# Performance work log

Measured on AMD Instinct MI355X. Metric: run time of the kernel, lower is better.

Reference implementation:

```python
import jax, jax.numpy as jnp
import numpy as np

N = 200000
C = 256
RATIO = 0.5
K = max(int(N * RATIO), 1)  # 100000 clusters kept


def setup_inputs() -> dict:
    key = jax.random.key(0)
    k1, k2, k3, k4 = jax.random.split(key, 4)
    x = jax.random.normal(k1, (N, C), dtype=jnp.float32)
    edge_index = jax.random.randint(k2, (2, N), 0, N, dtype=jnp.int32)  # E == N (source requires it)
    batch = jnp.zeros((N,), dtype=jnp.int32)
    # nn.Linear(C, 1): weight [1, C] -> flattened to [C]; bias [1] -> scalar
    w = jax.random.normal(k3, (C,), dtype=jnp.float32) * (1.0 / np.sqrt(C))
    b = jax.random.normal(k4, (1,), dtype=jnp.float32) * 0.01
    return {"x": x, "edge_index": edge_index, "batch": batch, "w": w, "b": b}


def reference(x, edge_index, batch, w, b):
    # scores = tanh(Linear(x)) over nodes: [N]
    scores = jnp.tanh(x @ w + b[0])
    # top-k node selection (torch uses sorted=False; ordering within topk is unspecified,
    # we use lax.top_k's sorted-descending order deterministically)
    _, perm = jax.lax.top_k(scores, K)  # [K] int32
    x_pool = x[perm]                    # [K, C]
    # mask is True for NON-selected nodes (as in the source)
    mask = jnp.ones((N,), dtype=bool).at[perm].set(False)
    # exactly N-K True entries (perm indices are distinct) -> static shape
    keep = jnp.nonzero(mask, size=N - K)[0]  # positions into edge rows (E == N)
    # relabel map: old node id -> new pooled id (0 for dropped nodes, as in source)
    new_mask = jnp.zeros((N,), dtype=jnp.int32).at[perm].set(jnp.arange(K, dtype=jnp.int32))
    ei = new_mask[edge_index[0][keep]]
    ej = new_mask[edge_index[1][keep]]
    edge_index_pool = jnp.stack([ei, ej], axis=0)  # [2, N-K]
    batch_pool = batch[perm]
    return (x_pool, edge_index_pool, perm, batch_pool, scores[perm])
```

## Files before the change

kernel.cpp:

```cpp
#include <hip/hip_runtime.h>

typedef unsigned long long u64;
typedef unsigned int u32;

#define NN 200000
#define CC 256
#define KK 100000
#define TILE 2048
#define NB ((NN + TILE - 1) / TILE)

#define OFF_X     0
#define OFF_E0    25600000
#define OFF_E1    25700000
#define OFF_PERM  25800000
#define OFF_BATCH 25900000
#define OFF_SC    26000000

__device__ __forceinline__ u32 key_of_f32(float s) {
    u32 b = __float_as_uint(s);
    u32 u = b ^ ((b & 0x80000000u) ? 0xFFFFFFFFu : 0x80000000u);
    return ~u;
}

__device__ __forceinline__ float xla_tanhf(float x) {
    const float kMax = (float)7.90531110763549805;
    float xc = fminf(fmaxf(x, -kMax), kMax);
    float x2 = __fmul_rn(xc, xc);
    float p = (float)-2.76076847742355e-16;
    p = __fadd_rn(__fmul_rn(p, x2), (float)2.00018790482477e-13);
    p = __fadd_rn(__fmul_rn(p, x2), (float)-8.60467152213735e-11);
    p = __fadd_rn(__fmul_rn(p, x2), (float)5.12229709037114e-08);
    p = __fadd_rn(__fmul_rn(p, x2), (float)1.48572235717979e-05);
    p = __fadd_rn(__fmul_rn(p, x2), (float)6.37261928875436e-04);
    p = __fadd_rn(__fmul_rn(p, x2), (float)4.89352455891786e-03);
    float num = __fmul_rn(xc, p);
    float q = (float)1.19825839466702e-06;
    q = __fadd_rn(__fmul_rn(q, x2), (float)1.18534705686654e-04);
    q = __fadd_rn(__fmul_rn(q, x2), (float)2.26843463243900e-03);
    q = __fadd_rn(__fmul_rn(q, x2), (float)4.89352518554385e-03);
    float t = __fdiv_rn(num, q);
    return (fabsf(x) < 0.0004f) ? x : t;
}

__global__ void score_kernel(const float* __restrict__ x, const float* __restrict__ w,
                             const float* __restrict__ b, u32* __restrict__ keys,
                             u32* __restrict__ vals, float* __restrict__ scoreF) {
    int i = (int)(blockIdx.x * blockDim.x + threadIdx.x);
    if (i >= NN) return;
    const float4* row = (const float4*)(x + (size_t)i * CC);
    const float4* wv  = (const float4*)w;
    float c0 = 0.f, c1 = 0.f, c2 = 0.f, c3 = 0.f;
    float c4 = 0.f, c5 = 0.f, c6 = 0.f, c7 = 0.f;
#pragma unroll 8
    for (int t = 0; t < 32; ++t) {
        float4 a0 = row[2 * t], a1 = row[2 * t + 1];
        float4 w0 = wv[2 * t],  w1 = wv[2 * t + 1];
        c0 = __builtin_fmaf(a0.x, w0.x, c0);
        c1 = __builtin_fmaf(a0.y, w0.y, c1);
        c2 = __builtin_fmaf(a0.z, w0.z, c2);
        c3 = __builtin_fmaf(a0.w, w0.w, c3);
        c4 = __builtin_fmaf(a1.x, w1.x, c4);
        c5 = __builtin_fmaf(a1.y, w1.y, c5);
        c6 = __builtin_fmaf(a1.z, w1.z, c6);
        c7 = __builtin_fmaf(a1.w, w1.w, c7);
    }
    float d0 = __fadd_rn(c0, c1);
    float d1 = __fadd_rn(c2, c3);
    float d2 = __fadd_rn(c4, c5);
    float d3 = __fadd_rn(c6, c7);
    float e0 = __fadd_rn(d0, d1);
    float e1 = __fadd_rn(d2, d3);
    float dot = __fadd_rn(e0, e1);
    float z = __fadd_rn(dot, b[0]);
    float s = xla_tanhf(z);
    keys[i]   = key_of_f32(s);
    keys[i]   = key_of_f32(s);
    vals[i]   = (u32)i;
    scoreF[i] = s;
}


__global__ void radix_count(const u32* __restrict__ keys, int shift,
                            u32* __restrict__ counts , int n) {
    __shared__ u32 hist[256];
    hist[threadIdx.x] = 0;
    __syncthreads();
    int wv = threadIdx.x >> 6, lane = threadIdx.x & 63;
    int base = blockIdx.x * TILE + wv * 512;
#pragma unroll
    for (int e = 0; e < 8; ++e) {
        int i = base + e * 64 + lane;
        if (i < n) {
            u32 d = (keys[i] >> shift) & 255u;
            atomicAdd(&hist[d], 1u);
        }
    }
    __syncthreads();
    counts[blockIdx.x * 256 + threadIdx.x] = hist[threadIdx.x];
}

template<bool ZMARK>
__global__ void radix_scatter(const u32* __restrict__ keysIn, const u32* __restrict__ valsIn,
                              u32* __restrict__ keysOut, u32* __restrict__ valsOut,
                              int shift, const u32* __restrict__ counts,
                              int* __restrict__ mark, int n) {
    __shared__ u32 waveCnt[4][256];
    __shared__ u32 scanbuf[256];
    __shared__ u32 tot[256];
    int tid = threadIdx.x;
    int wv = tid >> 6, lane = tid & 63;
    int myb = blockIdx.x;

    u32 myprefix = 0, total = 0;
#pragma unroll 7
    for (int bb = 0; bb < NB; ++bb) {
        u32 c = counts[bb * 256 + tid];
        if (bb < myb) myprefix += c;
        total += c;
    }
    tot[tid] = total;
    scanbuf[tid] = total;
#pragma unroll
    for (int w = 0; w < 4; ++w) waveCnt[w][tid] = 0;
    __syncthreads();
#pragma unroll
    for (int off = 1; off < 256; off <<= 1) {
        u32 v = (tid >= off) ? scanbuf[tid - off] : 0u;
        __syncthreads();
        scanbuf[tid] += v;
        __syncthreads();
    }
    u32 globalBase = (scanbuf[tid] - tot[tid]) + myprefix;

    int base = myb * TILE + wv * 512;
    u32 k[8];
    u64 peers[8];
    u32 dg[8];
    int valid[8];
#pragma unroll
    for (int e = 0; e < 8; ++e) {
        int i = base + e * 64 + lane;
        valid[e] = (i < n);
        k[e] = valid[e] ? keysIn[i] : 0u;
        dg[e] = (k[e] >> shift) & 255u;
        if (ZMARK && valid[e]) mark[i] = 0;
    }
#pragma unroll
    for (int e = 0; e < 8; ++e) {
        u64 mask = __ballot(valid[e]);
#pragma unroll
        for (int bit = 0; bit < 8; ++bit) {
            u64 bal = __ballot(valid[e] && ((dg[e] >> bit) & 1u));
            mask &= ((dg[e] >> bit) & 1u) ? bal : ~bal;
        }
        peers[e] = mask;
        if (valid[e]) {
            u64 lower = mask & ((1ull << lane) - 1ull);
            if (lower == 0ull)
                waveCnt[wv][dg[e]] += (u32)__popcll(mask);
        }
    }
    __syncthreads();
    {
        u32 r = globalBase;
#pragma unroll
        for (int w = 0; w < 4; ++w) { u32 c = waveCnt[w][tid]; waveCnt[w][tid] = r; r += c; }
    }
    __syncthreads();
#pragma unroll
    for (int e = 0; e < 8; ++e) {
        if (valid[e]) {
            u64 mask = peers[e];
            u64 lower = mask & ((1ull << lane) - 1ull);
            u32 rk = (u32)__popcll(lower);
            u32 pos = waveCnt[wv][dg[e]] + rk;
            keysOut[pos] = k[e];
            valsOut[pos] = valsIn[base + e * 64 + lane];
            if (lower == 0ull) waveCnt[wv][dg[e]] += (u32)__popcll(mask);
        }
    }
}


__global__ void gather_sel(const float* __restrict__ x, const u32* __restrict__ vals,
                           const float* __restrict__ scoreF, const int* __restrict__ batch,
                           float* __restrict__ out, int* __restrict__ mark) {
    int kI = (int)((blockIdx.x * blockDim.x + threadIdx.x) >> 6);
    int lane = threadIdx.x & 63;
    if (kI >= KK) return;
    u32 idx = vals[kI];
    const float4* src = (const float4*)(x + (size_t)idx * CC);
    float4* dst = (float4*)(out + OFF_X + (size_t)kI * CC);
    dst[lane] = src[lane];
    if (lane == 0) {
        out[OFF_PERM + kI]  = (float)idx;
        out[OFF_SC + kI]    = scoreF[idx];
        out[OFF_BATCH + kI] = (float)batch[idx];
        mark[idx] = kI + 1;
    }
}

__global__ void keep_count(const int* __restrict__ mark, u32* __restrict__ blockCnt) {
    __shared__ u32 wsum[4];
    int wv = threadIdx.x >> 6, lane = threadIdx.x & 63;
    if (threadIdx.x < 4) wsum[threadIdx.x] = 0;
    __syncthreads();
    int base = blockIdx.x * TILE + wv * 512;
    u32 cnt = 0;
#pragma unroll
    for (int e = 0; e < 8; ++e) {
        int i = base + e * 64 + lane;
        if (i < NN && mark[i] == 0) cnt++;
    }
#pragma unroll
    for (int off = 32; off > 0; off >>= 1) cnt += __shfl_xor(cnt, off);
    if (lane == 0) wsum[wv] = cnt;
    __syncthreads();
    if (threadIdx.x == 0) blockCnt[blockIdx.x] = wsum[0] + wsum[1] + wsum[2] + wsum[3];
}

__global__ void edge_scatter(const int* __restrict__ mark, const int* __restrict__ e0,
                             const int* __restrict__ e1, const u32* __restrict__ blockCnt,
                             float* __restrict__ out) {
    __shared__ u32 wbase[4];
    __shared__ u32 wsum2[4];
    int tid = threadIdx.x, wv = tid >> 6, lane = tid & 63, myb = blockIdx.x;
    int base = myb * TILE + wv * 512;

    u32 v = (tid < myb) ? blockCnt[tid] : 0u;
#pragma unroll
    for (int off = 32; off > 0; off >>= 1) v += __shfl_xor(v, off);
    if (lane == 0) wsum2[wv] = v;

    bool flag[8];
    u32 cnt = 0;
#pragma unroll
    for (int e = 0; e < 8; ++e) {
        int i = base + e * 64 + lane;
        flag[e] = (i < NN) && (mark[i] == 0);
        if (flag[e]) cnt++;
    }
    u32 wc = cnt;
#pragma unroll
    for (int off = 32; off > 0; off >>= 1) wc += __shfl_xor(wc, off);
    if (lane == 0) wbase[wv] = wc;
    __syncthreads();
    u32 bOff = wsum2[0] + wsum2[1] + wsum2[2] + wsum2[3];
    if (tid == 0) {
        u32 r = bOff;
#pragma unroll
        for (int w = 0; w < 4; ++w) { u32 c = wbase[w]; wbase[w] = r; r += c; }
    }
    __syncthreads();
    u32 run = wbase[wv];
#pragma unroll
    for (int e = 0; e < 8; ++e) {
        u64 bal = __ballot(flag[e]);
        if (flag[e]) {
            u32 pos = run + (u32)__popcll(bal & ((1ull << lane) - 1ull));
            int i = base + e * 64 + lane;
            int a = mark[e0[i]] - 1; if (a < 0) a = 0;
            int c = mark[e1[i]] - 1; if (c < 0) c = 0;
            out[OFF_E0 + pos] = (float)a;
            out[OFF_E1 + pos] = (float)c;
        }
        run += (u32)__popcll(bal);
    }
}

extern "C" void kernel_launch(void* const* d_in, const int* in_sizes, int n_in,
                              void* d_out, int out_size, void* d_ws, size_t ws_size,
                              hipStream_t stream) {
    (void)in_sizes; (void)n_in; (void)out_size; (void)ws_size;
    const float* x     = (const float*)d_in[0];
    const int*   ei    = (const int*)d_in[1];
    const int*   batch = (const int*)d_in[2];
    const float* w     = (const float*)d_in[3];
    const float* b     = (const float*)d_in[4];
    float* out = (float*)d_out;

    char* p = (char*)d_ws;
    u32* keys0 = (u32*)p;            p += (size_t)NN * 4;
    u32* keys1 = (u32*)p;            p += (size_t)NN * 4;
    u32* vals0 = (u32*)p;            p += (size_t)NN * 4;
    u32* vals1 = (u32*)p;            p += (size_t)NN * 4;
    float* scoreF = (float*)p;       p += (size_t)NN * 4;
    int* mark = (int*)p;             p += (size_t)NN * 4;
    u32* counts = (u32*)p;           p += (size_t)NB * 256 * 4;
    u32* blockCnt = (u32*)p;         p += (size_t)NB * 4;

    score_kernel<<<(NN + 255) / 256, 256, 0, stream>>>(x, w, b, keys0, vals0, scoreF);

    radix_count<<<NB, 256, 0, stream>>>(keys0, 0, counts, NN);
    radix_scatter<false><<<NB, 256, 0, stream>>>(keys0, vals0, keys1, vals1, 0, counts,
                                                 nullptr, NN);
    radix_count<<<NB, 256, 0, stream>>>(keys1, 8, counts, NN);
    radix_scatter<false><<<NB, 256, 0, stream>>>(keys1, vals1, keys0, vals0, 8, counts,
                                                 nullptr, NN);
    radix_count<<<NB, 256, 0, stream>>>(keys0, 16, counts, NN);
    radix_scatter<false><<<NB, 256, 0, stream>>>(keys0, vals0, keys1, vals1, 16, counts,
                                                 nullptr, NN);
    radix_count<<<NB, 256, 0, stream>>>(keys1, 24, counts, NN);
    radix_scatter<true><<<NB, 256, 0, stream>>>(keys1, vals1, keys0, vals0, 24, counts,
                                                mark, NN);

    gather_sel<<<KK * 64 / 256, 256, 0, stream>>>(x, vals0, scoreF, batch, out, mark);
    keep_count<<<NB, 256, 0, stream>>>(mark, blockCnt);
    edge_scatter<<<NB, 256, 0, stream>>>(mark, ei, ei + NN, blockCnt, out);
}
```

Measured before the change: 178.8 us.

## Stage radix scatter through LDS for coalesced global writes

```diff
diff --git a/kernel.cpp b/kernel.cpp
--- a/kernel.cpp
+++ b/kernel.cpp
@@ -74,7 +74,6 @@
     float z = __fadd_rn(dot, b[0]);
     float s = xla_tanhf(z);
     keys[i]   = key_of_f32(s);
-    keys[i]   = key_of_f32(s);
     vals[i]   = (u32)i;
     scoreF[i] = s;
 }
@@ -107,6 +106,10 @@
     __shared__ u32 waveCnt[4][256];
     __shared__ u32 scanbuf[256];
     __shared__ u32 tot[256];
+    __shared__ u32 gb[256];
+    __shared__ u32 lstart[256];
+    __shared__ u32 kLDS[TILE];
+    __shared__ u32 vLDS[TILE];
     int tid = threadIdx.x;
     int wv = tid >> 6, lane = tid & 63;
     int myb = blockIdx.x;
@@ -130,10 +133,11 @@
         scanbuf[tid] += v;
         __syncthreads();
     }
-    u32 globalBase = (scanbuf[tid] - tot[tid]) + myprefix;
+    gb[tid] = (scanbuf[tid] - tot[tid]) + myprefix;
 
     int base = myb * TILE + wv * 512;
     u32 k[8];
+    u32 vv[8];
     u64 peers[8];
     u32 dg[8];
     int valid[8];
@@ -142,6 +146,7 @@
         int i = base + e * 64 + lane;
         valid[e] = (i < n);
         k[e] = valid[e] ? keysIn[i] : 0u;
+        vv[e] = valid[e] ? valsIn[i] : 0u;
         dg[e] = (k[e] >> shift) & 255u;
         if (ZMARK && valid[e]) mark[i] = 0;
     }
@@ -162,7 +167,22 @@
     }
     __syncthreads();
     {
-        u32 r = globalBase;
+        u32 bh = waveCnt[0][tid] + waveCnt[1][tid] + waveCnt[2][tid] + waveCnt[3][tid];
+        scanbuf[tid] = bh;
+        tot[tid] = bh;
+    }
+    __syncthreads();
+#pragma unroll
+    for (int off = 1; off < 256; off <<= 1) {
+        u32 v = (tid >= off) ? scanbuf[tid - off] : 0u;
+        __syncthreads();
+        scanbuf[tid] += v;
+        __syncthreads();
+    }
+    lstart[tid] = scanbuf[tid] - tot[tid];
+    __syncthreads();
+    {
+        u32 r = lstart[tid];
 #pragma unroll
         for (int w = 0; w < 4; ++w) { u32 c = waveCnt[w][tid]; waveCnt[w][tid] = r; r += c; }
     }
@@ -173,10 +193,23 @@
             u64 mask = peers[e];
             u64 lower = mask & ((1ull << lane) - 1ull);
             u32 rk = (u32)__popcll(lower);
-            u32 pos = waveCnt[wv][dg[e]] + rk;
-            keysOut[pos] = k[e];
-            valsOut[pos] = valsIn[base + e * 64 + lane];
+            u32 lpos = waveCnt[wv][dg[e]] + rk;
+            kLDS[lpos] = k[e];
+            vLDS[lpos] = vv[e];
             if (lower == 0ull) waveCnt[wv][dg[e]] += (u32)__popcll(mask);
+        }
+    }
+    __syncthreads();
+    int vcnt = n - myb * TILE; if (vcnt > TILE) vcnt = TILE;
+#pragma unroll
+    for (int e = 0; e < 8; ++e) {
+        int p = e * 256 + tid;
+        if (p < vcnt) {
+            u32 kk = kLDS[p];
+            u32 d = (kk >> shift) & 255u;
+            u32 gpos = gb[d] + ((u32)p - lstart[d]);
+            keysOut[gpos] = kk;
+            valsOut[gpos] = vLDS[p];
         }
     }
 }
```

Result: faster. 175.0 us (-2.1%).
